# Optimization experiments

Measured on AMD Instinct MI355X. Metric: run time of the kernel, lower is better.

Reference implementation:

```python
import jax, jax.numpy as jnp
import numpy as np

B, S, H = 2, 2048, 2048
NH, NKV, HD = 16, 4, 128
SCALING = HD ** -0.5


def rotate_half(x):
    x1, x2 = jnp.split(x, 2, axis=-1)
    return jnp.concatenate((-x2, x1), axis=-1)


def apply_rope(t, cos, sin):
    # t: [B, nh, S, HD]; cos/sin: [B, S, HD] -> unsqueeze head dim
    c = cos[:, None, :, :]
    s = sin[:, None, :, :]
    return t * c + rotate_half(t) * s


def setup_inputs() -> dict:
    key = jax.random.key(0)
    k1, k2, k3, k4, k5 = jax.random.split(key, 5)
    hidden_states = jax.random.normal(k1, (B, S, H), dtype=jnp.float32)
    # real RoPE tables
    inv_freq = 1.0 / (10000.0 ** (jnp.arange(0, HD, 2, dtype=jnp.float32) / HD))
    pos = jnp.arange(S, dtype=jnp.float32)
    freqs = jnp.einsum('s,d->sd', pos, inv_freq)              # [S, HD/2]
    emb = jnp.concatenate((freqs, freqs), axis=-1)            # [S, HD]
    cos = jnp.broadcast_to(jnp.cos(emb)[None], (B, S, HD))
    sin = jnp.broadcast_to(jnp.sin(emb)[None], (B, S, HD))
    # additive causal mask [B, 1, S, S]
    causal = jnp.triu(jnp.full((S, S), -1e9, dtype=jnp.float32), k=1)
    attention_mask = jnp.broadcast_to(causal[None, None], (B, 1, S, S))
    sc = 0.02
    wq = jax.random.normal(k2, (NH * HD, H), dtype=jnp.float32) * sc
    wk = jax.random.normal(k3, (NKV * HD, H), dtype=jnp.float32) * sc
    wv = jax.random.normal(k4, (NKV * HD, H), dtype=jnp.float32) * sc
    wo = jax.random.normal(k5, (H, NH * HD), dtype=jnp.float32) * sc
    return {"hidden_states": hidden_states, "cos": cos, "sin": sin,
            "attention_mask": attention_mask, "wq": wq, "wk": wk, "wv": wv, "wo": wo}


def reference(hidden_states, cos, sin, attention_mask, wq, wk, wv, wo):
    x = hidden_states
    # fused-style QKV projections (nn.Linear: x @ W.T), split heads -> [B, nh, S, HD]
    q = (x @ wq.T).reshape(B, S, NH, HD).transpose(0, 2, 1, 3)
    k = (x @ wk.T).reshape(B, S, NKV, HD).transpose(0, 2, 1, 3)
    v = (x @ wv.T).reshape(B, S, NKV, HD).transpose(0, 2, 1, 3)
    q = apply_rope(q, cos, sin)
    k = apply_rope(k, cos, sin)
    # GQA: repeat KV heads (repeat_kv)
    n_rep = NH // NKV
    k = jnp.repeat(k, n_rep, axis=1)
    v = jnp.repeat(v, n_rep, axis=1)
    scores = jnp.einsum('bhqd,bhkd->bhqk', q, k) * SCALING + attention_mask
    attn = jax.nn.softmax(scores.astype(jnp.float32), axis=-1).astype(q.dtype)
    out = jnp.einsum('bhqk,bhkd->bhqd', attn, v)
    out = out.transpose(0, 2, 1, 3).reshape(B, S, NH * HD)
    out = out @ wo.T
    return (out, attn)
```

## Files before the change

kernel.cpp:

```cpp
#include <hip/hip_runtime.h>
#include <cstdint>
#include <cstddef>

typedef __bf16 bf16;
typedef __attribute__((ext_vector_type(8))) __bf16 bf16x8;
typedef __attribute__((ext_vector_type(4))) __bf16 bf16x4;
typedef __attribute__((ext_vector_type(4))) float f32x4;

constexpr int B_ = 2, S_ = 2048, H_ = 2048, NH_ = 16, NKV_ = 4, HD_ = 128;
constexpr float SCALE_ = 0.08838834764831845f;

#define GLDS16(g, l)                                                        \
  __builtin_amdgcn_global_load_lds(                                         \
      (const __attribute__((address_space(1))) void*)(g),                   \
      (__attribute__((address_space(3))) void*)(l), 16, 0, 0)

#define VMCNT0 asm volatile("s_waitcnt vmcnt(0)" ::: "memory")
#define BAR __builtin_amdgcn_s_barrier()

__device__ inline void nt_store4(float* p, f32x4 v) {
  __builtin_nontemporal_store(v, (f32x4*)p);
}

__global__ void cvt_all(const float* __restrict__ hs, const float* __restrict__ wq,
                        const float* __restrict__ wk, const float* __restrict__ wv,
                        const float* __restrict__ wo, bf16* __restrict__ xb,
                        bf16* __restrict__ w3b, bf16* __restrict__ wob) {
  const int stride = gridDim.x * blockDim.x;
  for (int i = blockIdx.x * blockDim.x + threadIdx.x; i < 4718592; i += stride) {
    const float4* s; bf16x4* d; int j;
    if (i < 2097152)      { s = (const float4*)hs; d = (bf16x4*)xb;            j = i; }
    else if (i < 3145728) { s = (const float4*)wq; d = (bf16x4*)w3b;           j = i - 2097152; }
    else if (i < 3407872) { s = (const float4*)wk; d = (bf16x4*)w3b + 1048576; j = i - 3145728; }
    else if (i < 3670016) { s = (const float4*)wv; d = (bf16x4*)w3b + 1310720; j = i - 3407872; }
    else                  { s = (const float4*)wo; d = (bf16x4*)wob;           j = i - 3670016; }
    float4 v = s[j];
    bf16x4 o;
    o[0] = (bf16)v.x; o[1] = (bf16)v.y; o[2] = (bf16)v.z; o[3] = (bf16)v.w;
    d[j] = o;
  }
}

template <int EPI>
__global__ __launch_bounds__(256) void gemm_bt(const bf16* __restrict__ A,
                                               const bf16* __restrict__ Bm, int K,
                                               bf16* __restrict__ qb, bf16* __restrict__ kb,
                                               bf16* __restrict__ vtb, float* __restrict__ Cout) {
  __shared__ __align__(16) bf16 As[128 * 64];
  __shared__ __align__(16) bf16 Bs[128 * 64];
  const int tid = threadIdx.x;
  const int lane = tid & 63;
  const int wid = tid >> 6;
  const int fid = blockIdx.y * 32 + blockIdx.x;
  const int nwg = gridDim.y * 32;
  const int swz = (fid & 7) * (nwg >> 3) + (fid >> 3);
  const int m0 = (swz & 31) * 128;
  const int n0 = (swz >> 5) * 128;
  const int wm = (wid >> 1) * 64, wn = (wid & 1) * 64;
  const int r = lane & 15, g = lane >> 4;
  f32x4 acc[4][4] = {};

#pragma unroll 1
  for (int kt = 0; kt < K; kt += 64) {
    __syncthreads();
#pragma unroll
    for (int i = 0; i < 4; ++i) {
      int cb = wid * 256 + i * 64;
      int c64 = cb + lane;
      int row = c64 >> 3, cs = (c64 & 7) ^ (row & 7);
      GLDS16(A + (size_t)(m0 + row) * K + kt + cs * 8, As + cb * 8);
      GLDS16(Bm + (size_t)(n0 + row) * K + kt + cs * 8, Bs + cb * 8);
    }
    VMCNT0;
    __syncthreads();
#pragma unroll
    for (int ks = 0; ks < 2; ++ks) {
      bf16x8 af[4], bfr[4];
#pragma unroll
      for (int fm = 0; fm < 4; ++fm)
        af[fm] = *(const bf16x8*)(As + (wm + fm * 16 + r) * 64 + (((ks * 4 + g) ^ (r & 7)) << 3));
#pragma unroll
      for (int fn = 0; fn < 4; ++fn)
        bfr[fn] = *(const bf16x8*)(Bs + (wn + fn * 16 + r) * 64 + (((ks * 4 + g) ^ (r & 7)) << 3));
#pragma unroll
      for (int fm = 0; fm < 4; ++fm)
#pragma unroll
        for (int fn = 0; fn < 4; ++fn)
          acc[fm][fn] = __builtin_amdgcn_mfma_f32_16x16x32_bf16(af[fm], bfr[fn], acc[fm][fn], 0, 0, 0);
    }
  }

#pragma unroll
  for (int fm = 0; fm < 4; ++fm)
#pragma unroll
    for (int fn = 0; fn < 4; ++fn)
#pragma unroll
      for (int rr = 0; rr < 4; ++rr) {
        int mm = m0 + wm + fm * 16 + g * 4 + rr;
        int nn = n0 + wn + fn * 16 + r;
        float v = acc[fm][fn][rr];
        if (EPI == 1) {
          Cout[(size_t)mm * 2048 + nn] = v;
        } else {
          int b = mm >> 11, s = mm & (S_ - 1);
          int d = nn & 127;
          if (nn < 2048) {
            int hh = nn >> 7;
            qb[(((size_t)b * NH_ + hh) * S_ + s) * HD_ + d] = (bf16)v;
          } else if (nn < 2560) {
            int hh = (nn - 2048) >> 7;
            kb[(((size_t)b * NKV_ + hh) * S_ + s) * HD_ + d] = (bf16)v;
          } else {
            int hh = (nn - 2560) >> 7;
            vtb[(((size_t)b * NKV_ + hh) * HD_ + d) * S_ + s] = (bf16)v;
          }
        }
      }
}

__global__ void rope_k_kernel(bf16* __restrict__ kb, const float* __restrict__ cosp,
                              const float* __restrict__ sinp) {
  const int NK = B_ * NKV_ * S_;
  int t = blockIdx.x * blockDim.x + threadIdx.x;
  if (t >= NK * 8) return;
  const int oct = t & 7, rid = t >> 3;
  bf16* base = kb + (size_t)rid * HD_;
  const int s = rid & (S_ - 1);
  const int b = rid >> 13;
  const int d = oct * 8;
  const float* cp = cosp + ((size_t)b * S_ + s) * HD_ + d;
  const float* sp = sinp + ((size_t)b * S_ + s) * HD_ + d;
  float4 c0 = *(const float4*)cp, c1 = *(const float4*)(cp + 4);
  float4 s0 = *(const float4*)sp, s1 = *(const float4*)(sp + 4);
  float cc[8] = {c0.x, c0.y, c0.z, c0.w, c1.x, c1.y, c1.z, c1.w};
  float ss[8] = {s0.x, s0.y, s0.z, s0.w, s1.x, s1.y, s1.z, s1.w};
  bf16x8 x1 = *(const bf16x8*)(base + d);
  bf16x8 x2 = *(const bf16x8*)(base + d + 64);
  bf16x8 o1, o2;
#pragma unroll
  for (int i = 0; i < 8; ++i) {
    float a = (float)x1[i], bb = (float)x2[i];
    o1[i] = (bf16)(a * cc[i] - bb * ss[i]);
    o2[i] = (bf16)(bb * cc[i] + a * ss[i]);
  }
  *(bf16x8*)(base + d) = o1;
  *(bf16x8*)(base + d + 64) = o2;
}

__global__ __launch_bounds__(256, 2) void attn_kernel(const bf16* __restrict__ qb,
                                                      const bf16* __restrict__ kb,
                                                      const bf16* __restrict__ vtb,
                                                      const float* __restrict__ cosp,
                                                      const float* __restrict__ sinp,
                                                      bf16* __restrict__ aob,
                                                      float* __restrict__ attn_out) {
  __shared__ __align__(16) bf16 Ks[64 * 128];
  __shared__ __align__(16) bf16 Vs[128 * 64];
  __shared__ __align__(16) bf16 Ps[64 * 64];
  const int x7 = blockIdx.x & 7;
  const int k = blockIdx.x >> 3;
  const int qt = (k < 32) ? (31 - k) : (k - 32);
  const int g2 = x7 + ((k >> 5) << 3);
  const int b = g2 >> 3;
  const int kh = (g2 >> 1) & 3;
  const int hp = g2 & 1;
  const int h0 = kh * 4 + hp * 2;
  const int q0 = qt * 64;
  const int nt = qt + 1;
  const int tid = threadIdx.x, lane = tid & 63, wid = tid >> 6;
  const int r = lane & 15, g = lane >> 4;

  const bf16* kbase = kb + ((size_t)b * NKV_ + kh) * S_ * HD_;
  const bf16* vbase = vtb + ((size_t)b * NKV_ + kh) * (size_t)HD_ * S_;
  size_t arow0[2];
#pragma unroll
  for (int hh = 0; hh < 2; ++hh)
    arow0[hh] = ((size_t)(b * NH_ + h0 + hh) * S_ + q0) * S_;

  auto stageK = [&](int kt) {
#pragma unroll
    for (int i = 0; i < 4; ++i) {
      int base = i * 256 + wid * 64;
      int idx = base + lane;
      int row = idx >> 4, ch = (idx & 15) ^ (row & 7);
      GLDS16(kbase + (size_t)(kt * 64 + row) * HD_ + ch * 8, Ks + base * 8);
    }
  };
  auto stageV = [&](int kt) {
#pragma unroll
    for (int i = 0; i < 4; ++i) {
      int base = i * 256 + wid * 64;
      int idx = base + lane;
      int row = idx >> 3, ch = (idx & 7) ^ (row & 7);
      GLDS16(vbase + (size_t)row * S_ + kt * 64 + ch * 8, Vs + base * 8);
    }
  };

  bf16x8 qreg[2][4];
  {
    const int srow = q0 + wid * 16 + r;
    const float* cp = cosp + ((size_t)b * S_ + srow) * HD_;
    const float* sp = sinp + ((size_t)b * S_ + srow) * HD_;
    float cc[2][8], ss[2][8];
#pragma unroll
    for (int hf = 0; hf < 2; ++hf) {
      const int d0 = hf * 32 + g * 8;
      float4 ca = *(const float4*)(cp + d0), cb2 = *(const float4*)(cp + d0 + 4);
      float4 sa = *(const float4*)(sp + d0), sb2 = *(const float4*)(sp + d0 + 4);
      cc[hf][0] = ca.x; cc[hf][1] = ca.y; cc[hf][2] = ca.z; cc[hf][3] = ca.w;
      cc[hf][4] = cb2.x; cc[hf][5] = cb2.y; cc[hf][6] = cb2.z; cc[hf][7] = cb2.w;
      ss[hf][0] = sa.x; ss[hf][1] = sa.y; ss[hf][2] = sa.z; ss[hf][3] = sa.w;
      ss[hf][4] = sb2.x; ss[hf][5] = sb2.y; ss[hf][6] = sb2.z; ss[hf][7] = sb2.w;
    }
#pragma unroll
    for (int hh = 0; hh < 2; ++hh) {
      const bf16* qsrc = qb + ((size_t)(b * NH_ + h0 + hh) * S_ + q0) * HD_;
#pragma unroll
      for (int ks = 0; ks < 4; ++ks)
        qreg[hh][ks] = *(const bf16x8*)(qsrc + (wid * 16 + r) * HD_ + ks * 32 + g * 8);
#pragma unroll
      for (int hf = 0; hf < 2; ++hf) {
        bf16x8 lo = qreg[hh][hf], hi = qreg[hh][hf + 2];
#pragma unroll
        for (int i = 0; i < 8; ++i) {
          float a = (float)lo[i], bb = (float)hi[i];
          qreg[hh][hf][i] = (bf16)(a * cc[hf][i] - bb * ss[hf][i]);
          qreg[hh][hf + 2][i] = (bf16)(bb * cc[hf][i] + a * ss[hf][i]);
        }
      }
    }
  }

  const int nzero = 62 - 2 * qt;
  int zc = 0;

  float lsum[2] = {0.f, 0.f};
#pragma unroll 1
  for (int kt = 0; kt < nt; ++kt) {
    __syncthreads();
    stageK(kt);
    VMCNT0;
    __syncthreads();
#pragma unroll
    for (int zi = 0; zi < 2; ++zi) {
      if (zc < nzero) {
        int hh = (zc >= 31 - qt) ? 1 : 0;
        int ktz = qt + 1 + (hh ? zc - (31 - qt) : zc);
        float* zdst = attn_out + arow0[hh] + ktz * 64;
        f32x4 z = {0.f, 0.f, 0.f, 0.f};
#pragma unroll
        for (int i = 0; i < 4; ++i) {
          int idx = i * 256 + tid;
          nt_store4(zdst + (size_t)(idx >> 4) * S_ + (idx & 15) * 4, z);
        }
        ++zc;
      }
    }
#pragma unroll
    for (int hh = 0; hh < 2; ++hh) {
      f32x4 sacc[4] = {};
      __builtin_amdgcn_s_setprio(1);
#pragma unroll
      for (int ks = 0; ks < 4; ++ks)
#pragma unroll
        for (int fn = 0; fn < 4; ++fn) {
          bf16x8 kk = *(const bf16x8*)(Ks + (fn * 16 + r) * 128 + (((ks * 4 + g) ^ (r & 7)) << 3));
          sacc[fn] = __builtin_amdgcn_mfma_f32_16x16x32_bf16(kk, qreg[hh][ks], sacc[fn], 0, 0, 0);
        }
      __builtin_amdgcn_s_setprio(0);
      float ts = 0.f;
      if (kt == nt - 1) {
#pragma unroll
        for (int fn = 0; fn < 4; ++fn)
#pragma unroll
          for (int rr = 0; rr < 4; ++rr) {
            bool msk = (fn * 16 + g * 4 + rr) > (wid * 16 + r);
            ts += msk ? 0.f : __expf(sacc[fn][rr] * SCALE_);
          }
      } else {
#pragma unroll
        for (int fn = 0; fn < 4; ++fn)
#pragma unroll
          for (int rr = 0; rr < 4; ++rr) ts += __expf(sacc[fn][rr] * SCALE_);
      }
      ts += __shfl_xor(ts, 16);
      ts += __shfl_xor(ts, 32);
      lsum[hh] += ts;
    }
  }
  float rl[2] = {1.0f / lsum[0], 1.0f / lsum[1]};

  f32x4 oacc[2][8] = {};
#pragma unroll 1
  for (int kt = 0; kt < nt; ++kt) {
    const int k0 = kt * 64;
    __syncthreads();
    stageK(kt);
    stageV(kt);
    VMCNT0;
    __syncthreads();
    const bool last = (kt == nt - 1);
#pragma unroll
    for (int hh = 0; hh < 2; ++hh) {
      f32x4 sacc[4] = {};
      __builtin_amdgcn_s_setprio(1);
#pragma unroll
      for (int ks = 0; ks < 4; ++ks)
#pragma unroll
        for (int fn = 0; fn < 4; ++fn) {
          bf16x8 kk = *(const bf16x8*)(Ks + (fn * 16 + r) * 128 + (((ks * 4 + g) ^ (r & 7)) << 3));
          sacc[fn] = __builtin_amdgcn_mfma_f32_16x16x32_bf16(kk, qreg[hh][ks], sacc[fn], 0, 0, 0);
        }
      __builtin_amdgcn_s_setprio(0);
      const int prow = (wid * 16 + r) * 64;
#pragma unroll
      for (int fn = 0; fn < 4; ++fn) {
        f32x4 pv4;
        bf16x4 pk;
#pragma unroll
        for (int rr = 0; rr < 4; ++rr) {
          bool msk = last && ((fn * 16 + g * 4 + rr) > (wid * 16 + r));
          float f = msk ? 0.f : __expf(sacc[fn][rr] * SCALE_) * rl[hh];
          pv4[rr] = f;
          pk[rr] = (bf16)f;
        }
        nt_store4(attn_out + arow0[hh] + (size_t)(wid * 16 + r) * S_ + k0 + fn * 16 + g * 4, pv4);
        *(bf16x4*)(&Ps[prow + ((((fn << 1) | (g >> 1)) ^ (r & 7)) << 3) + ((g & 1) << 2)]) = pk;
      }
      __builtin_amdgcn_s_setprio(1);
#pragma unroll
      for (int ks = 0; ks < 2; ++ks) {
        bf16x8 pa = *(const bf16x8*)(&Ps[prow + (((ks * 4 + g) ^ (r & 7)) << 3)]);
#pragma unroll
        for (int fn = 0; fn < 8; ++fn) {
          bf16x8 vv = *(const bf16x8*)(Vs + (fn * 16 + r) * 64 + (((ks * 4 + g) ^ (r & 7)) << 3));
          oacc[hh][fn] = __builtin_amdgcn_mfma_f32_16x16x32_bf16(pa, vv, oacc[hh][fn], 0, 0, 0);
        }
      }
      __builtin_amdgcn_s_setprio(0);
    }
  }

#pragma unroll
  for (int hh = 0; hh < 2; ++hh)
#pragma unroll
    for (int fn = 0; fn < 8; ++fn)
#pragma unroll
      for (int rr = 0; rr < 4; ++rr) {
        int q = q0 + wid * 16 + g * 4 + rr;
        aob[((size_t)b * S_ + q) * 2048 + (h0 + hh) * HD_ + fn * 16 + r] = (bf16)oacc[hh][fn][rr];
      }

#pragma unroll 1
  for (; zc < nzero; ++zc) {
    int hh = (zc >= 31 - qt) ? 1 : 0;
    int ktz = qt + 1 + (hh ? zc - (31 - qt) : zc);
    float* zdst = attn_out + arow0[hh] + ktz * 64;
    f32x4 z = {0.f, 0.f, 0.f, 0.f};
#pragma unroll
    for (int i = 0; i < 4; ++i) {
      int idx = i * 256 + tid;
      nt_store4(zdst + (size_t)(idx >> 4) * S_ + (idx & 15) * 4, z);
    }
  }
}

extern "C" void kernel_launch(void* const* d_in, const int* in_sizes, int n_in,
                              void* d_out, int out_size, void* d_ws, size_t ws_size,
                              hipStream_t stream) {
  const float* hidden = (const float*)d_in[0];
  const float* cosp = (const float*)d_in[1];
  const float* sinp = (const float*)d_in[2];
  const float* wq = (const float*)d_in[4];
  const float* wk = (const float*)d_in[5];
  const float* wv = (const float*)d_in[6];
  const float* wo = (const float*)d_in[7];
  float* out = (float*)d_out;
  float* attn = out + (size_t)B_ * S_ * H_;

  char* ws = (char*)d_ws;
  bf16* xb  = (bf16*)(ws);
  bf16* w3b = (bf16*)(ws + (16ull << 20));
  bf16* wob = (bf16*)(ws + (28ull << 20));
  bf16* qb  = (bf16*)(ws + (36ull << 20));
  bf16* kb  = (bf16*)(ws + (52ull << 20));
  bf16* vtb = (bf16*)(ws + (56ull << 20));
  bf16* aob = (bf16*)(ws + (60ull << 20));

  cvt_all<<<2048, 256, 0, stream>>>(hidden, wq, wk, wv, wo, xb, w3b, wob);
  gemm_bt<0><<<dim3(32, 24), 256, 0, stream>>>(xb, w3b, 2048, qb, kb, vtb, nullptr);
  rope_k_kernel<<<512, 256, 0, stream>>>(kb, cosp, sinp);
  attn_kernel<<<512, 256, 0, stream>>>(qb, kb, vtb, cosp, sinp, aob, attn);
  gemm_bt<1><<<dim3(32, 16), 256, 0, stream>>>(aob, wob, 2048, nullptr, nullptr, nullptr, out);
}
```

Before: 340.9 us.

## Double-buffer K/V tiles in LDS with prefetch of next tile

K and V shared-memory tiles become two buffers. The next tile is fetched with global_load_lds while MFMAs run on the current one, and there is one barrier per iteration instead of two syncthreads with a full wait. This is meant to hide global-to-LDS load latency in both the row-sum pass and the output pass. The zero-filling of masked attention tiles moves out of the first loop to the kernel tail. The second loop relies on vmcnt(8) counting the outstanding attention-output stores, and the doubled LDS footprint (about 72KB per block) could limit occupancy.

```diff
diff --git a/kernel.cpp b/kernel.cpp
--- a/kernel.cpp
+++ b/kernel.cpp
@@ -16,6 +16,8 @@
       (__attribute__((address_space(3))) void*)(l), 16, 0, 0)
 
 #define VMCNT0 asm volatile("s_waitcnt vmcnt(0)" ::: "memory")
+#define VMCNT8 asm volatile("s_waitcnt vmcnt(8)" ::: "memory")
+#define SCHED0 __builtin_amdgcn_sched_barrier(0)
 #define BAR __builtin_amdgcn_s_barrier()
 
 __device__ inline void nt_store4(float* p, f32x4 v) {
@@ -154,8 +156,8 @@
                                                       const float* __restrict__ sinp,
                                                       bf16* __restrict__ aob,
                                                       float* __restrict__ attn_out) {
-  __shared__ __align__(16) bf16 Ks[64 * 128];
-  __shared__ __align__(16) bf16 Vs[128 * 64];
+  __shared__ __align__(16) bf16 Ks[2][64 * 128];
+  __shared__ __align__(16) bf16 Vs[2][128 * 64];
   __shared__ __align__(16) bf16 Ps[64 * 64];
   const int x7 = blockIdx.x & 7;
   const int k = blockIdx.x >> 3;
@@ -177,22 +179,22 @@
   for (int hh = 0; hh < 2; ++hh)
     arow0[hh] = ((size_t)(b * NH_ + h0 + hh) * S_ + q0) * S_;
 
-  auto stageK = [&](int kt) {
+  auto stageK = [&](int kt, int cc) {
 #pragma unroll
     for (int i = 0; i < 4; ++i) {
       int base = i * 256 + wid * 64;
       int idx = base + lane;
       int row = idx >> 4, ch = (idx & 15) ^ (row & 7);
-      GLDS16(kbase + (size_t)(kt * 64 + row) * HD_ + ch * 8, Ks + base * 8);
+      GLDS16(kbase + (size_t)(kt * 64 + row) * HD_ + ch * 8, &Ks[cc][base * 8]);
     }
   };
-  auto stageV = [&](int kt) {
+  auto stageV = [&](int kt, int cc) {
 #pragma unroll
     for (int i = 0; i < 4; ++i) {
       int base = i * 256 + wid * 64;
       int idx = base + lane;
       int row = idx >> 3, ch = (idx & 7) ^ (row & 7);
-      GLDS16(vbase + (size_t)row * S_ + kt * 64 + ch * 8, Vs + base * 8);
+      GLDS16(vbase + (size_t)row * S_ + kt * 64 + ch * 8, &Vs[cc][base * 8]);
     }
   };
 
@@ -231,31 +233,14 @@
     }
   }
 
-  const int nzero = 62 - 2 * qt;
-  int zc = 0;
-
   float lsum[2] = {0.f, 0.f};
+  stageK(0, 0);
+  VMCNT0; BAR;
+  int c = 0;
 #pragma unroll 1
   for (int kt = 0; kt < nt; ++kt) {
-    __syncthreads();
-    stageK(kt);
-    VMCNT0;
-    __syncthreads();
-#pragma unroll
-    for (int zi = 0; zi < 2; ++zi) {
-      if (zc < nzero) {
-        int hh = (zc >= 31 - qt) ? 1 : 0;
-        int ktz = qt + 1 + (hh ? zc - (31 - qt) : zc);
-        float* zdst = attn_out + arow0[hh] + ktz * 64;
-        f32x4 z = {0.f, 0.f, 0.f, 0.f};
-#pragma unroll
-        for (int i = 0; i < 4; ++i) {
-          int idx = i * 256 + tid;
-          nt_store4(zdst + (size_t)(idx >> 4) * S_ + (idx & 15) * 4, z);
-        }
-        ++zc;
-      }
-    }
+    const bool hn = (kt + 1 < nt);
+    if (hn) { stageK(kt + 1, c ^ 1); SCHED0; }
 #pragma unroll
     for (int hh = 0; hh < 2; ++hh) {
       f32x4 sacc[4] = {};
@@ -264,7 +249,7 @@
       for (int ks = 0; ks < 4; ++ks)
 #pragma unroll
         for (int fn = 0; fn < 4; ++fn) {
-          bf16x8 kk = *(const bf16x8*)(Ks + (fn * 16 + r) * 128 + (((ks * 4 + g) ^ (r & 7)) << 3));
+          bf16x8 kk = *(const bf16x8*)(&Ks[c][(fn * 16 + r) * 128 + (((ks * 4 + g) ^ (r & 7)) << 3)]);
           sacc[fn] = __builtin_amdgcn_mfma_f32_16x16x32_bf16(kk, qreg[hh][ks], sacc[fn], 0, 0, 0);
         }
       __builtin_amdgcn_s_setprio(0);
@@ -287,18 +272,22 @@
       ts += __shfl_xor(ts, 32);
       lsum[hh] += ts;
     }
+    if (hn) { VMCNT0; }
+    BAR;
+    c ^= 1;
   }
   float rl[2] = {1.0f / lsum[0], 1.0f / lsum[1]};
 
   f32x4 oacc[2][8] = {};
+  stageK(0, 0);
+  stageV(0, 0);
+  VMCNT0; BAR;
+  c = 0;
 #pragma unroll 1
   for (int kt = 0; kt < nt; ++kt) {
     const int k0 = kt * 64;
-    __syncthreads();
-    stageK(kt);
-    stageV(kt);
-    VMCNT0;
-    __syncthreads();
+    const bool hn = (kt + 1 < nt);
+    if (hn) { stageK(kt + 1, c ^ 1); stageV(kt + 1, c ^ 1); SCHED0; }
     const bool last = (kt == nt - 1);
 #pragma unroll
     for (int hh = 0; hh < 2; ++hh) {
@@ -308,7 +297,7 @@
       for (int ks = 0; ks < 4; ++ks)
 #pragma unroll
         for (int fn = 0; fn < 4; ++fn) {
-          bf16x8 kk = *(const bf16x8*)(Ks + (fn * 16 + r) * 128 + (((ks * 4 + g) ^ (r & 7)) << 3));
+          bf16x8 kk = *(const bf16x8*)(&Ks[c][(fn * 16 + r) * 128 + (((ks * 4 + g) ^ (r & 7)) << 3)]);
           sacc[fn] = __builtin_amdgcn_mfma_f32_16x16x32_bf16(kk, qreg[hh][ks], sacc[fn], 0, 0, 0);
         }
       __builtin_amdgcn_s_setprio(0);
@@ -333,12 +322,15 @@
         bf16x8 pa = *(const bf16x8*)(&Ps[prow + (((ks * 4 + g) ^ (r & 7)) << 3)]);
 #pragma unroll
         for (int fn = 0; fn < 8; ++fn) {
-          bf16x8 vv = *(const bf16x8*)(Vs + (fn * 16 + r) * 64 + (((ks * 4 + g) ^ (r & 7)) << 3));
+          bf16x8 vv = *(const bf16x8*)(&Vs[c][(fn * 16 + r) * 64 + (((ks * 4 + g) ^ (r & 7)) << 3)]);
           oacc[hh][fn] = __builtin_amdgcn_mfma_f32_16x16x32_bf16(pa, vv, oacc[hh][fn], 0, 0, 0);
         }
       }
       __builtin_amdgcn_s_setprio(0);
     }
+    if (hn) { VMCNT8; }
+    BAR;
+    c ^= 1;
   }
 
 #pragma unroll
@@ -351,16 +343,17 @@
         aob[((size_t)b * S_ + q) * 2048 + (h0 + hh) * HD_ + fn * 16 + r] = (bf16)oacc[hh][fn][rr];
       }
 
+  const int nzero = 62 - 2 * qt;
 #pragma unroll 1
-  for (; zc < nzero; ++zc) {
-    int hh = (zc >= 31 - qt) ? 1 : 0;
-    int ktz = qt + 1 + (hh ? zc - (31 - qt) : zc);
+  for (int z = 0; z < nzero; ++z) {
+    int hh = (z >= 31 - qt) ? 1 : 0;
+    int ktz = qt + 1 + (hh ? z - (31 - qt) : z);
     float* zdst = attn_out + arow0[hh] + ktz * 64;
-    f32x4 z = {0.f, 0.f, 0.f, 0.f};
+    f32x4 zv = {0.f, 0.f, 0.f, 0.f};
 #pragma unroll
     for (int i = 0; i < 4; ++i) {
       int idx = i * 256 + tid;
-      nt_store4(zdst + (size_t)(idx >> 4) * S_ + (idx & 15) * 4, z);
+      nt_store4(zdst + (size_t)(idx >> 4) * S_ + (idx & 15) * 4, zv);
     }
   }
 }
```

After: 340.5 us. About the same (-0.1%).

## Widen attention KV tile to 128 keys and defer zero-fill to end

Applied to the files above, without the earlier changes.

The attention kernel now processes 128 keys per iteration instead of 64, with larger K/V/P shared-memory tiles and XOR swizzles widened to 16 chunks. This halves the number of loop iterations and barriers in both passes, and each staged K/V tile feeds more MFMA work. The zero-filling of masked-out attention blocks is no longer interleaved with the first pass. All of it now runs after the output write, which may reduce overlap of stores with compute. Shared memory grows to about 80KB per block, which can limit the 2-blocks-per-CU launch bound, and odd query tiles do extra masked work in the last tile.

```diff
diff --git a/kernel.cpp b/kernel.cpp
--- a/kernel.cpp
+++ b/kernel.cpp
@@ -154,9 +154,9 @@
                                                       const float* __restrict__ sinp,
                                                       bf16* __restrict__ aob,
                                                       float* __restrict__ attn_out) {
-  __shared__ __align__(16) bf16 Ks[64 * 128];
-  __shared__ __align__(16) bf16 Vs[128 * 64];
-  __shared__ __align__(16) bf16 Ps[64 * 64];
+  __shared__ __align__(16) bf16 Ks[128 * 128];
+  __shared__ __align__(16) bf16 Vs[128 * 128];
+  __shared__ __align__(16) bf16 Ps[64 * 128];
   const int x7 = blockIdx.x & 7;
   const int k = blockIdx.x >> 3;
   const int qt = (k < 32) ? (31 - k) : (k - 32);
@@ -166,7 +166,7 @@
   const int hp = g2 & 1;
   const int h0 = kh * 4 + hp * 2;
   const int q0 = qt * 64;
-  const int nt = qt + 1;
+  const int nt = (qt + 2) >> 1;
   const int tid = threadIdx.x, lane = tid & 63, wid = tid >> 6;
   const int r = lane & 15, g = lane >> 4;
 
@@ -179,20 +179,20 @@
 
   auto stageK = [&](int kt) {
 #pragma unroll
-    for (int i = 0; i < 4; ++i) {
+    for (int i = 0; i < 8; ++i) {
       int base = i * 256 + wid * 64;
       int idx = base + lane;
-      int row = idx >> 4, ch = (idx & 15) ^ (row & 7);
-      GLDS16(kbase + (size_t)(kt * 64 + row) * HD_ + ch * 8, Ks + base * 8);
+      int row = idx >> 4, ch = (idx & 15) ^ (row & 15);
+      GLDS16(kbase + (size_t)(kt * 128 + row) * HD_ + ch * 8, Ks + base * 8);
     }
   };
   auto stageV = [&](int kt) {
 #pragma unroll
-    for (int i = 0; i < 4; ++i) {
+    for (int i = 0; i < 8; ++i) {
       int base = i * 256 + wid * 64;
       int idx = base + lane;
-      int row = idx >> 3, ch = (idx & 7) ^ (row & 7);
-      GLDS16(vbase + (size_t)row * S_ + kt * 64 + ch * 8, Vs + base * 8);
+      int row = idx >> 4, ch = (idx & 15) ^ (row & 15);
+      GLDS16(vbase + (size_t)row * S_ + kt * 128 + ch * 8, Vs + base * 8);
     }
   };
 
@@ -231,9 +231,6 @@
     }
   }
 
-  const int nzero = 62 - 2 * qt;
-  int zc = 0;
-
   float lsum[2] = {0.f, 0.f};
 #pragma unroll 1
   for (int kt = 0; kt < nt; ++kt) {
@@ -241,45 +238,32 @@
     stageK(kt);
     VMCNT0;
     __syncthreads();
-#pragma unroll
-    for (int zi = 0; zi < 2; ++zi) {
-      if (zc < nzero) {
-        int hh = (zc >= 31 - qt) ? 1 : 0;
-        int ktz = qt + 1 + (hh ? zc - (31 - qt) : zc);
-        float* zdst = attn_out + arow0[hh] + ktz * 64;
-        f32x4 z = {0.f, 0.f, 0.f, 0.f};
-#pragma unroll
-        for (int i = 0; i < 4; ++i) {
-          int idx = i * 256 + tid;
-          nt_store4(zdst + (size_t)(idx >> 4) * S_ + (idx & 15) * 4, z);
-        }
-        ++zc;
-      }
-    }
+    const bool last = (kt == nt - 1);
+    const int k0 = kt * 128;
 #pragma unroll
     for (int hh = 0; hh < 2; ++hh) {
-      f32x4 sacc[4] = {};
+      f32x4 sacc[8] = {};
       __builtin_amdgcn_s_setprio(1);
 #pragma unroll
       for (int ks = 0; ks < 4; ++ks)
 #pragma unroll
-        for (int fn = 0; fn < 4; ++fn) {
-          bf16x8 kk = *(const bf16x8*)(Ks + (fn * 16 + r) * 128 + (((ks * 4 + g) ^ (r & 7)) << 3));
+        for (int fn = 0; fn < 8; ++fn) {
+          bf16x8 kk = *(const bf16x8*)(Ks + (fn * 16 + r) * 128 + (((ks * 4 + g) ^ r) << 3));
           sacc[fn] = __builtin_amdgcn_mfma_f32_16x16x32_bf16(kk, qreg[hh][ks], sacc[fn], 0, 0, 0);
         }
       __builtin_amdgcn_s_setprio(0);
       float ts = 0.f;
-      if (kt == nt - 1) {
-#pragma unroll
-        for (int fn = 0; fn < 4; ++fn)
+      if (last) {
+#pragma unroll
+        for (int fn = 0; fn < 8; ++fn)
 #pragma unroll
           for (int rr = 0; rr < 4; ++rr) {
-            bool msk = (fn * 16 + g * 4 + rr) > (wid * 16 + r);
+            bool msk = (k0 + fn * 16 + g * 4 + rr) > (q0 + wid * 16 + r);
             ts += msk ? 0.f : __expf(sacc[fn][rr] * SCALE_);
           }
       } else {
 #pragma unroll
-        for (int fn = 0; fn < 4; ++fn)
+        for (int fn = 0; fn < 8; ++fn)
 #pragma unroll
           for (int rr = 0; rr < 4; ++rr) ts += __expf(sacc[fn][rr] * SCALE_);
       }
@@ -293,47 +277,47 @@
   f32x4 oacc[2][8] = {};
 #pragma unroll 1
   for (int kt = 0; kt < nt; ++kt) {
-    const int k0 = kt * 64;
     __syncthreads();
     stageK(kt);
     stageV(kt);
     VMCNT0;
     __syncthreads();
+    const int k0 = kt * 128;
     const bool last = (kt == nt - 1);
 #pragma unroll
     for (int hh = 0; hh < 2; ++hh) {
-      f32x4 sacc[4] = {};
+      f32x4 sacc[8] = {};
       __builtin_amdgcn_s_setprio(1);
 #pragma unroll
       for (int ks = 0; ks < 4; ++ks)
 #pragma unroll
-        for (int fn = 0; fn < 4; ++fn) {
-          bf16x8 kk = *(const bf16x8*)(Ks + (fn * 16 + r) * 128 + (((ks * 4 + g) ^ (r & 7)) << 3));
+        for (int fn = 0; fn < 8; ++fn) {
+          bf16x8 kk = *(const bf16x8*)(Ks + (fn * 16 + r) * 128 + (((ks * 4 + g) ^ r) << 3));
           sacc[fn] = __builtin_amdgcn_mfma_f32_16x16x32_bf16(kk, qreg[hh][ks], sacc[fn], 0, 0, 0);
         }
       __builtin_amdgcn_s_setprio(0);
-      const int prow = (wid * 16 + r) * 64;
-#pragma unroll
-      for (int fn = 0; fn < 4; ++fn) {
+      const int prow = (wid * 16 + r) * 128;
+#pragma unroll
+      for (int fn = 0; fn < 8; ++fn) {
         f32x4 pv4;
         bf16x4 pk;
 #pragma unroll
         for (int rr = 0; rr < 4; ++rr) {
-          bool msk = last && ((fn * 16 + g * 4 + rr) > (wid * 16 + r));
+          bool msk = last && ((k0 + fn * 16 + g * 4 + rr) > (q0 + wid * 16 + r));
           float f = msk ? 0.f : __expf(sacc[fn][rr] * SCALE_) * rl[hh];
           pv4[rr] = f;
           pk[rr] = (bf16)f;
         }
         nt_store4(attn_out + arow0[hh] + (size_t)(wid * 16 + r) * S_ + k0 + fn * 16 + g * 4, pv4);
-        *(bf16x4*)(&Ps[prow + ((((fn << 1) | (g >> 1)) ^ (r & 7)) << 3) + ((g & 1) << 2)]) = pk;
+        *(bf16x4*)(&Ps[prow + ((((fn << 1) | (g >> 1)) ^ r) << 3) + ((g & 1) << 2)]) = pk;
       }
       __builtin_amdgcn_s_setprio(1);
 #pragma unroll
-      for (int ks = 0; ks < 2; ++ks) {
-        bf16x8 pa = *(const bf16x8*)(&Ps[prow + (((ks * 4 + g) ^ (r & 7)) << 3)]);
+      for (int ks = 0; ks < 4; ++ks) {
+        bf16x8 pa = *(const bf16x8*)(&Ps[prow + (((ks * 4 + g) ^ r) << 3)]);
 #pragma unroll
         for (int fn = 0; fn < 8; ++fn) {
-          bf16x8 vv = *(const bf16x8*)(Vs + (fn * 16 + r) * 64 + (((ks * 4 + g) ^ (r & 7)) << 3));
+          bf16x8 vv = *(const bf16x8*)(Vs + (fn * 16 + r) * 128 + (((ks * 4 + g) ^ r) << 3));
           oacc[hh][fn] = __builtin_amdgcn_mfma_f32_16x16x32_bf16(pa, vv, oacc[hh][fn], 0, 0, 0);
         }
       }
@@ -351,16 +335,17 @@
         aob[((size_t)b * S_ + q) * 2048 + (h0 + hh) * HD_ + fn * 16 + r] = (bf16)oacc[hh][fn][rr];
       }
 
+  const int z0 = 2 * nt;
 #pragma unroll 1
-  for (; zc < nzero; ++zc) {
-    int hh = (zc >= 31 - qt) ? 1 : 0;
-    int ktz = qt + 1 + (hh ? zc - (31 - qt) : zc);
+  for (int zi = 0; zi < 2 * (32 - z0); ++zi) {
+    int hh = (zi >= 32 - z0) ? 1 : 0;
+    int ktz = z0 + (hh ? zi - (32 - z0) : zi);
     float* zdst = attn_out + arow0[hh] + ktz * 64;
-    f32x4 z = {0.f, 0.f, 0.f, 0.f};
+    f32x4 zv = {0.f, 0.f, 0.f, 0.f};
 #pragma unroll
     for (int i = 0; i < 4; ++i) {
       int idx = i * 256 + tid;
-      nt_store4(zdst + (size_t)(idx >> 4) * S_ + (idx & 15) * 4, z);
+      nt_store4(zdst + (size_t)(idx >> 4) * S_ + (idx & 15) * 4, zv);
     }
   }
 }
```

After: 332.4 us (median of 2 runs). 1.03x faster.
